# Kernel optimization log

Measured on AMD Instinct MI355X. Metric: run time of the kernel, lower is better.

Reference implementation:

```python
import jax, jax.numpy as jnp
import numpy as np

B, S, D, F, E = 4, 1024, 768, 3072, 8


def setup_inputs() -> dict:
    key = jax.random.key(0)
    k0, k1, k2, k3 = jax.random.split(key, 4)
    hidden_states = jax.random.normal(k0, (B, S, D), dtype=jnp.float32)
    w_router = jax.random.normal(k1, (D, E), dtype=jnp.float32) * 0.02
    w1 = jax.random.normal(k2, (E, D, F), dtype=jnp.float32) * 0.02
    b1 = jnp.zeros((E, F), dtype=jnp.float32)
    w2 = jax.random.normal(k3, (E, F, D), dtype=jnp.float32) * 0.02
    b2 = jnp.zeros((E, D), dtype=jnp.float32)
    return {"hidden_states": hidden_states, "w_router": w_router,
            "w1": w1, "b1": b1, "w2": w2, "b2": b2}


def reference(hidden_states, w_router, w1, b1, w2, b2):
    # Switch-style top-1 router: logits -> softmax -> one-hot mask + max prob
    router_logits = jnp.einsum("bsd,de->bse", hidden_states, w_router)
    router_probs_full = jax.nn.softmax(router_logits, axis=-1)
    expert_index = jnp.argmax(router_probs_full, axis=-1)            # [B,S] int
    router_probs = jnp.max(router_probs_full, axis=-1, keepdims=True)  # [B,S,1]
    router_mask = jax.nn.one_hot(expert_index, E, dtype=hidden_states.dtype)  # [B,S,E]

    # Dispatch/compute/combine: each token goes to exactly one expert FFN.
    # Loop over the small fixed expert set (E=8), combine via the one-hot mask;
    # math is identical to the gather -> expert FFN -> scatter of the original.
    out = jnp.zeros_like(hidden_states)
    for e in range(E):
        h = jax.nn.relu(jnp.einsum("bsd,df->bsf", hidden_states, w1[e]) + b1[e])
        h = jnp.einsum("bsf,fd->bsd", h, w2[e]) + b2[e]
        out = out + router_mask[..., e:e + 1] * h

    hidden_out = router_probs * out  # scale by top-1 router prob, as in original
    return hidden_out, router_logits, expert_index
```

## Files before the change

kernel.cpp:

```cpp
#include <hip/hip_runtime.h>
#include <hip/hip_bf16.h>

#define T_TOK 4096
#define DIM   768
#define FF    3072
#define NE    8
#define MAXTILES 48

typedef __attribute__((ext_vector_type(8))) short bf16x8;
typedef __attribute__((ext_vector_type(4))) short bf16x4;
typedef __attribute__((ext_vector_type(4))) float f32x4;
typedef __attribute__((ext_vector_type(2))) float f32x2;

typedef __attribute__((address_space(1))) void gvoid_t;
typedef __attribute__((address_space(3))) void lvoid_t;

__device__ __forceinline__ void g2l16(const void* g, void* l) {
    __builtin_amdgcn_global_load_lds((gvoid_t*)(void*)g, (lvoid_t*)l, 16, 0, 0);
}

#define WAIT_VM0() __builtin_amdgcn_s_waitcnt(0x0F70)
#define WAIT_VM4() __builtin_amdgcn_s_waitcnt(0x0F74)
#define RAW_BARRIER() asm volatile("s_barrier" ::: "memory")

__device__ __forceinline__ unsigned short f2bf(float f) {
    union { float f; unsigned int u; } v; v.f = f;
    unsigned int u = v.u;
    u += 0x7FFFu + ((u >> 16) & 1u);
    return (unsigned short)(u >> 16);
}

__device__ __forceinline__ bf16x8 pack8(f32x4 a, f32x4 b) {
    bf16x8 r;
    r[0] = (short)f2bf(a[0]); r[1] = (short)f2bf(a[1]);
    r[2] = (short)f2bf(a[2]); r[3] = (short)f2bf(a[3]);
    r[4] = (short)f2bf(b[0]); r[5] = (short)f2bf(b[1]);
    r[6] = (short)f2bf(b[2]); r[7] = (short)f2bf(b[3]);
    return r;
}

__global__ __launch_bounds__(256) void k_router(
    const float* __restrict__ x, const float* __restrict__ wr,
    float* __restrict__ out_logits, float* __restrict__ out_eidx,
    float* __restrict__ probs, int* __restrict__ eidx_i,
    int* __restrict__ counts, int* __restrict__ bucket)
{
    int tok  = (blockIdx.x * 256 + threadIdx.x) >> 6;
    int lane = threadIdx.x & 63;
    if (tok >= T_TOK) return;
    const float* xr = x + (size_t)tok * DIM;
    float acc[NE];
    #pragma unroll
    for (int e = 0; e < NE; e++) acc[e] = 0.f;
    #pragma unroll
    for (int j = 0; j < DIM / 64; j++) {
        int d = j * 64 + lane;
        float xv = xr[d];
        const float* wrow = wr + (size_t)d * NE;
        #pragma unroll
        for (int e = 0; e < NE; e++) acc[e] += xv * wrow[e];
    }
    #pragma unroll
    for (int e = 0; e < NE; e++) {
        #pragma unroll
        for (int off = 32; off >= 1; off >>= 1)
            acc[e] += __shfl_xor(acc[e], off);
    }
    if (lane == 0) {
        float mx = acc[0]; int mi = 0;
        #pragma unroll
        for (int e = 1; e < NE; e++) if (acc[e] > mx) { mx = acc[e]; mi = e; }
        float se = 0.f;
        #pragma unroll
        for (int e = 0; e < NE; e++) se += __expf(acc[e] - mx);
        #pragma unroll
        for (int e = 0; e < NE; e++) out_logits[(size_t)tok * NE + e] = acc[e];
        out_eidx[tok] = (float)mi;
        eidx_i[tok] = mi;
        probs[tok] = 1.f / se;
        int pos = atomicAdd(&counts[mi], 1);
        bucket[mi * T_TOK + pos] = tok;
    }
}

__global__ void k_compact(const int* __restrict__ counts, int* __restrict__ offsets,
                          int* __restrict__ bucket, int* __restrict__ sorted)
{
    __shared__ int soff[NE + 1];
    if (threadIdx.x == 0) {
        int s = 0;
        for (int e = 0; e < NE; e++) { soff[e] = s; s += counts[e]; }
        soff[NE] = s;
        for (int e = 0; e <= NE; e++) offsets[e] = soff[e];
    }
    __syncthreads();
    for (int e = 0; e < NE; e++) {
        int c = counts[e], o = soff[e];
        for (int i = threadIdx.x; i < c; i += blockDim.x)
            sorted[o + i] = bucket[e * T_TOK + i];
    }
    __syncthreads();
    if (threadIdx.x == 0) {
        int nt = 0;
        for (int e = 0; e < NE; e++) {
            int c = counts[e];
            for (int t = 0; t * 128 < c && nt < MAXTILES; t++)
                bucket[nt++] = (e << 8) | t;
        }
        for (int i = nt; i < MAXTILES; i++) bucket[i] = -1;
    }
}

__global__ __launch_bounds__(256) void k_xconv(
    const float* __restrict__ x, unsigned short* __restrict__ Xb)
{
    int g0 = (blockIdx.x * 256 + threadIdx.x) * 8;
    if (g0 >= T_TOK * DIM) return;
    f32x4 a = *(const f32x4*)(x + g0);
    f32x4 b = *(const f32x4*)(x + g0 + 4);
    *(bf16x8*)(Xb + g0) = pack8(a, b);
}

__global__ __launch_bounds__(256) void k_tconv(
    const float* __restrict__ in, unsigned short* __restrict__ out, int R, int C)
{
    const size_t es = (size_t)R * C;
    in  += blockIdx.z * es;
    out += blockIdx.z * es;
    const int c0 = blockIdx.x * 64, r0 = blockIdx.y * 64;
    __shared__ unsigned short t[64][72];
    const int tr = threadIdx.x >> 2, tc = (threadIdx.x & 3) * 16;
    const float* src = in + (size_t)(r0 + tr) * C + c0 + tc;
    f32x4 v0 = *(const f32x4*)(src);
    f32x4 v1 = *(const f32x4*)(src + 4);
    f32x4 v2 = *(const f32x4*)(src + 8);
    f32x4 v3 = *(const f32x4*)(src + 12);
    const int xb = (tc >> 4) & 3;
    const int pr = (((tr >> 3) ^ xb) & 7) * 8 + (tr & 7);
    #pragma unroll
    for (int j = 0; j < 4; j++) {
        t[tc + j][pr]      = f2bf(v0[j]);
        t[tc + 4 + j][pr]  = f2bf(v1[j]);
        t[tc + 8 + j][pr]  = f2bf(v2[j]);
        t[tc + 12 + j][pr] = f2bf(v3[j]);
    }
    __syncthreads();
    const int oc = threadIdx.x >> 2, orr = (threadIdx.x & 3) * 16;
    const int rx = (oc >> 4) & 3;
    const int p0 = ((((orr >> 3) + 0) ^ rx) & 7) * 8;
    const int p1 = ((((orr >> 3) + 1) ^ rx) & 7) * 8;
    bf16x8 o0 = *(const bf16x8*)&t[oc][p0];
    bf16x8 o1 = *(const bf16x8*)&t[oc][p1];
    unsigned short* dst = out + (size_t)(c0 + oc) * R + r0 + orr;
    *(bf16x8*)(dst)     = o0;
    *(bf16x8*)(dst + 8) = o1;
}

__global__ __launch_bounds__(256) void k_fin(
    const float* __restrict__ P, const float* __restrict__ b2,
    const int* __restrict__ eidx, const float* __restrict__ probs,
    float* __restrict__ outh)
{
    const int tok = blockIdx.x;
    const float p = probs[tok];
    const int e = eidx[tok];
    const float* p0 = P + (size_t)tok * DIM;
    const float* p1 = p0 + (size_t)T_TOK * DIM;
    const float* p2 = p1 + (size_t)T_TOK * DIM;
    const float* br = b2 + e * DIM;
    float* o = outh + (size_t)tok * DIM;
    for (int d = threadIdx.x; d < DIM; d += 256)
        o[d] = p * (p0[d] + p1[d] + p2[d] + br[d]);
}

__global__ __launch_bounds__(256, 3) void k_gemm1(
    const unsigned short* __restrict__ Xb, const unsigned short* __restrict__ wt1,
    const float* __restrict__ b1, const int* __restrict__ sorted,
    const int* __restrict__ counts, const int* __restrict__ offsets,
    const int* __restrict__ tile_tab, unsigned short* __restrict__ Hbuf)
{
    const int tv = tile_tab[blockIdx.y];
    if (tv < 0) return;
    const int e  = tv >> 8;
    const int ti = tv & 255;
    const int cnt = counts[e];
    const int n0 = blockIdx.x * 128;
    const int off = offsets[e];
    const int rbase = ti * 128;
    const int tid = threadIdx.x, lane = tid & 63, wave = tid >> 6;
    const int wm = wave >> 1, wn = wave & 1;

    __shared__ unsigned short As[3][128][32];
    __shared__ unsigned short Bs[3][128][32];

    const int lr = lane >> 2;
    const int ls = (lane & 3) * 8;

    int r0 = rbase + wave * 32 + lr;        if (r0 >= cnt) r0 = rbase;
    int r1 = rbase + wave * 32 + 16 + lr;   if (r1 >= cnt) r1 = rbase;
    const unsigned short* aP0 = Xb + (size_t)sorted[off + r0] * DIM + ls;
    const unsigned short* aP1 = Xb + (size_t)sorted[off + r1] * DIM + ls;
    const unsigned short* wB  = wt1 + (size_t)e * FF * DIM;
    const unsigned short* bP0 = wB + (size_t)(n0 + wave * 32 + lr) * DIM + ls;
    const unsigned short* bP1 = wB + (size_t)(n0 + wave * 32 + 16 + lr) * DIM + ls;

    f32x4 acc[4][4];
    #pragma unroll
    for (int i = 0; i < 4; i++)
        #pragma unroll
        for (int j = 0; j < 4; j++) acc[i][j] = (f32x4)0.f;

    const int lrow = lane & 15, kq = lane >> 4;
    const int NIT = DIM / 32;

    g2l16(aP0, &As[0][wave * 32][0]);
    g2l16(aP1, &As[0][wave * 32 + 16][0]);
    g2l16(bP0, &Bs[0][wave * 32][0]);
    g2l16(bP1, &Bs[0][wave * 32 + 16][0]);
    __syncthreads();
    g2l16(aP0 + 32, &As[1][wave * 32][0]);
    g2l16(aP1 + 32, &As[1][wave * 32 + 16][0]);
    g2l16(bP0 + 32, &Bs[1][wave * 32][0]);
    g2l16(bP1 + 32, &Bs[1][wave * 32 + 16][0]);

    for (int it = 0; it < NIT; ++it) {
        const int buf = it % 3;
        if (it > 0) {
            WAIT_VM4();
            RAW_BARRIER();
        }
        if (it + 2 < NIT) {
            const int nb_ = (it + 2) % 3;
            const int ko = (it + 2) * 32;
            g2l16(aP0 + ko, &As[nb_][wave * 32][0]);
            g2l16(aP1 + ko, &As[nb_][wave * 32 + 16][0]);
            g2l16(bP0 + ko, &Bs[nb_][wave * 32][0]);
            g2l16(bP1 + ko, &Bs[nb_][wave * 32 + 16][0]);
        }
        bf16x8 af[4], bfv[4];
        #pragma unroll
        for (int i = 0; i < 4; i++)
            af[i] = *(const bf16x8*)&As[buf][wm * 64 + i * 16 + lrow][kq * 8];
        #pragma unroll
        for (int i = 0; i < 4; i++)
            bfv[i] = *(const bf16x8*)&Bs[buf][wn * 64 + i * 16 + lrow][kq * 8];
        #pragma unroll
        for (int mi = 0; mi < 4; mi++)
            #pragma unroll
            for (int ni = 0; ni < 4; ni++)
                acc[mi][ni] = __builtin_amdgcn_mfma_f32_16x16x32_bf16(
                    af[mi], bfv[ni], acc[mi][ni], 0, 0, 0);
    }

    const int quad = lane >> 4;
    #pragma unroll
    for (int ni = 0; ni < 4; ni++) {
        int gn = n0 + wn * 64 + ni * 16 + lrow;
        float bias = b1[e * FF + gn];
        #pragma unroll
        for (int mi = 0; mi < 4; mi++) {
            f32x4 v = acc[mi][ni];
            #pragma unroll
            for (int r = 0; r < 4; r++) {
                int ml = rbase + wm * 64 + mi * 16 + quad * 4 + r;
                if (ml < cnt) {
                    float h = v[r] + bias; h = h > 0.f ? h : 0.f;
                    Hbuf[(size_t)(off + ml) * FF + gn] = f2bf(h);
                }
            }
        }
    }
}

__global__ __launch_bounds__(256, 3) void k_gemm2(
    const unsigned short* __restrict__ Hbuf, const unsigned short* __restrict__ wt2,
    const int* __restrict__ sorted, const int* __restrict__ counts,
    const int* __restrict__ offsets, const int* __restrict__ tile_tab,
    float* __restrict__ Pbuf)
{
    const int tv = tile_tab[blockIdx.y];
    if (tv < 0) return;
    const int e  = tv >> 8;
    const int ti = tv & 255;
    const int cnt = counts[e];
    const int n0 = blockIdx.x * 128;
    const int kc = blockIdx.z;
    const int off = offsets[e];
    const int rbase = ti * 128;
    const int tid = threadIdx.x, lane = tid & 63, wave = tid >> 6;
    const int wm = wave >> 1, wn = wave & 1;

    __shared__ unsigned short As[3][128][32];
    __shared__ unsigned short Bs[3][128][32];
    __shared__ int s_tok[128];

    if (tid < 128) {
        int rr = rbase + tid; if (rr >= cnt) rr = rbase;
        s_tok[tid] = sorted[off + rr];
    }

    const int lr = lane >> 2, ls = (lane & 3) * 8;
    int r0 = rbase + wave * 32 + lr;        if (r0 >= cnt) r0 = rbase;
    int r1 = rbase + wave * 32 + 16 + lr;   if (r1 >= cnt) r1 = rbase;
    const unsigned short* aP0 = Hbuf + (size_t)(off + r0) * FF + kc * 1024 + ls;
    const unsigned short* aP1 = Hbuf + (size_t)(off + r1) * FF + kc * 1024 + ls;
    const unsigned short* wB  = wt2 + (size_t)e * DIM * FF;
    const unsigned short* bP0 = wB + (size_t)(n0 + wave * 32 + lr) * FF + kc * 1024 + ls;
    const unsigned short* bP1 = wB + (size_t)(n0 + wave * 32 + 16 + lr) * FF + kc * 1024 + ls;

    f32x4 acc[4][4];
    #pragma unroll
    for (int i = 0; i < 4; i++)
        #pragma unroll
        for (int j = 0; j < 4; j++) acc[i][j] = (f32x4)0.f;

    const int lrow = lane & 15, kq = lane >> 4;
    const int NIT = 1024 / 32;

    g2l16(aP0, &As[0][wave * 32][0]);
    g2l16(aP1, &As[0][wave * 32 + 16][0]);
    g2l16(bP0, &Bs[0][wave * 32][0]);
    g2l16(bP1, &Bs[0][wave * 32 + 16][0]);
    __syncthreads();
    g2l16(aP0 + 32, &As[1][wave * 32][0]);
    g2l16(aP1 + 32, &As[1][wave * 32 + 16][0]);
    g2l16(bP0 + 32, &Bs[1][wave * 32][0]);
    g2l16(bP1 + 32, &Bs[1][wave * 32 + 16][0]);

    for (int it = 0; it < NIT; ++it) {
        const int buf = it % 3;
        if (it > 0) {
            WAIT_VM4();
            RAW_BARRIER();
        }
        if (it + 2 < NIT) {
            const int nb_ = (it + 2) % 3;
            const int ko = (it + 2) * 32;
            g2l16(aP0 + ko, &As[nb_][wave * 32][0]);
            g2l16(aP1 + ko, &As[nb_][wave * 32 + 16][0]);
            g2l16(bP0 + ko, &Bs[nb_][wave * 32][0]);
            g2l16(bP1 + ko, &Bs[nb_][wave * 32 + 16][0]);
        }
        bf16x8 af[4], bfv[4];
        #pragma unroll
        for (int i = 0; i < 4; i++)
            af[i] = *(const bf16x8*)&As[buf][wm * 64 + i * 16 + lrow][kq * 8];
        #pragma unroll
        for (int i = 0; i < 4; i++)
            bfv[i] = *(const bf16x8*)&Bs[buf][wn * 64 + i * 16 + lrow][kq * 8];
        #pragma unroll
        for (int mi = 0; mi < 4; mi++)
            #pragma unroll
            for (int ni = 0; ni < 4; ni++)
                acc[mi][ni] = __builtin_amdgcn_mfma_f32_16x16x32_bf16(
                    af[mi], bfv[ni], acc[mi][ni], 0, 0, 0);
    }

    float* Pk = Pbuf + (size_t)kc * T_TOK * DIM;
    const int quad = lane >> 4;
    #pragma unroll
    for (int ni = 0; ni < 4; ni++) {
        int gn = n0 + wn * 64 + ni * 16 + lrow;
        #pragma unroll
        for (int mi = 0; mi < 4; mi++) {
            f32x4 v = acc[mi][ni];
            #pragma unroll
            for (int r = 0; r < 4; r++) {
                int mloc = wm * 64 + mi * 16 + quad * 4 + r;
                if (rbase + mloc < cnt) {
                    Pk[(size_t)s_tok[mloc] * DIM + gn] = v[r];
                }
            }
        }
    }
}

__global__ __launch_bounds__(256) void k_gather_fb(
    const float* __restrict__ x, const int* __restrict__ sorted,
    unsigned short* __restrict__ Xg)
{
    int g0 = (blockIdx.x * 256 + threadIdx.x) * 8;
    if (g0 >= T_TOK * DIM) return;
    int row = g0 / DIM, col = g0 - row * DIM;
    const float* src = x + (size_t)sorted[row] * DIM + col;
    f32x4 a = *(const f32x4*)(src);
    f32x4 b = *(const f32x4*)(src + 4);
    *(bf16x8*)(Xg + (size_t)row * DIM + col) = pack8(a, b);
}

__global__ __launch_bounds__(256, 3) void k_gemm1_fb(
    const unsigned short* __restrict__ Xg, const float* __restrict__ w1,
    const float* __restrict__ b1, const int* __restrict__ counts,
    const int* __restrict__ offsets, unsigned short* __restrict__ Hbuf)
{
    const int e   = blockIdx.y >> 5;
    const int ti  = blockIdx.y & 31;
    const int cnt = counts[e];
    if (ti * 128 >= cnt) return;
    const int n0    = blockIdx.x * 128;
    const int off   = offsets[e];
    const int rbase = ti * 128;
    const int rmax  = cnt - rbase - 1;
    const int tid   = threadIdx.x;
    const int lane  = tid & 63;
    const int wave  = tid >> 6;
    const int wm = wave >> 1, wn = wave & 1;
    __shared__ unsigned short As[128][72];
    __shared__ unsigned short Bs[128][72];
    const float* w1e = w1 + (size_t)e * DIM * FF;
    f32x4 acc[4][4];
    #pragma unroll
    for (int i = 0; i < 4; i++)
        #pragma unroll
        for (int j = 0; j < 4; j++) acc[i][j] = (f32x4)0.f;
    const int arow = tid >> 1, aseg = tid & 1;
    const int are  = (arow <= rmax) ? arow : 0;
    const unsigned short* abase = Xg + (size_t)(off + rbase + are) * DIM + aseg * 32;
    const int kb = tid >> 5, nb = tid & 31;
    const float* bbase = w1e + (size_t)kb * 8 * FF + n0 + nb * 4;
    bf16x8 aR[4];
    f32x4  bR[8];
    #pragma unroll
    for (int j = 0; j < 4; j++) aR[j] = *(const bf16x8*)(abase + j * 8);
    #pragma unroll
    for (int r = 0; r < 8; r++) bR[r] = *(const f32x4*)(bbase + (size_t)r * FF);
    const int lrow = lane & 15, kq = lane >> 4;
    for (int it = 0; it < DIM / 64; ++it) {
        __syncthreads();
        #pragma unroll
        for (int j = 0; j < 4; j++)
            *(bf16x8*)&As[arow][aseg * 32 + j * 8] = aR[j];
        #pragma unroll
        for (int j = 0; j < 4; j++) {
            bf16x8 c;
            #pragma unroll
            for (int r = 0; r < 8; r++) c[r] = (short)f2bf(bR[r][j]);
            *(bf16x8*)&Bs[nb * 4 + j][kb * 8] = c;
        }
        __syncthreads();
        if (it + 1 < DIM / 64) {
            const unsigned short* an = abase + (it + 1) * 64;
            #pragma unroll
            for (int j = 0; j < 4; j++) aR[j] = *(const bf16x8*)(an + j * 8);
            const float* bn = bbase + (size_t)(it + 1) * 64 * FF;
            #pragma unroll
            for (int r = 0; r < 8; r++) bR[r] = *(const f32x4*)(bn + (size_t)r * FF);
        }
        #pragma unroll
        for (int ks = 0; ks < 2; ks++) {
            bf16x8 af[4], bfr[4];
            #pragma unroll
            for (int i = 0; i < 4; i++)
                af[i] = *(const bf16x8*)&As[wm * 64 + i * 16 + lrow][ks * 32 + kq * 8];
            #pragma unroll
            for (int i = 0; i < 4; i++)
                bfr[i] = *(const bf16x8*)&Bs[wn * 64 + i * 16 + lrow][ks * 32 + kq * 8];
            #pragma unroll
            for (int mi = 0; mi < 4; mi++)
                #pragma unroll
                for (int ni = 0; ni < 4; ni++)
                    acc[mi][ni] = __builtin_amdgcn_mfma_f32_16x16x32_bf16(
                        af[mi], bfr[ni], acc[mi][ni], 0, 0, 0);
        }
    }
    const int quad = lane >> 4;
    #pragma unroll
    for (int ni = 0; ni < 4; ni++) {
        int gn = n0 + wn * 64 + ni * 16 + lrow;
        float bias = b1[e * FF + gn];
        #pragma unroll
        for (int mi = 0; mi < 4; mi++) {
            f32x4 v = acc[mi][ni];
            #pragma unroll
            for (int r = 0; r < 4; r++) {
                int ml = wm * 64 + mi * 16 + quad * 4 + r;
                if (rbase + ml < cnt) {
                    float h = v[r] + bias;
                    h = h > 0.f ? h : 0.f;
                    Hbuf[(size_t)(off + rbase + ml) * FF + gn] = f2bf(h);
                }
            }
        }
    }
}

__global__ __launch_bounds__(256, 4) void k_gemm2_fb(
    const unsigned short* __restrict__ Hbuf, const float* __restrict__ w2,
    const float* __restrict__ b2, const int* __restrict__ sorted,
    const int* __restrict__ counts, const int* __restrict__ offsets,
    const float* __restrict__ probs, float* __restrict__ outh)
{
    const int e   = blockIdx.y >> 5;
    const int ti  = blockIdx.y & 31;
    const int cnt = counts[e];
    if (ti * 128 >= cnt) return;
    const int n0    = blockIdx.x * 64;
    const int off   = offsets[e];
    const int rbase = ti * 128;
    const int rmax  = cnt - rbase - 1;
    const int tid   = threadIdx.x;
    const int lane  = tid & 63;
    const int wave  = tid >> 6;
    const int wm = wave >> 1, wn = wave & 1;
    __shared__ unsigned short As[128][72];
    __shared__ unsigned short Bs[64][72];
    __shared__ int   s_tok[128];
    __shared__ float s_prob[128];
    if (tid < 128) {
        int r = rbase + tid;
        int tk = sorted[off + ((r < cnt) ? r : rbase)];
        s_tok[tid]  = tk;
        s_prob[tid] = probs[tk];
    }
    const float* w2e = w2 + (size_t)e * FF * DIM;
    f32x4 acc[4][2];
    #pragma unroll
    for (int i = 0; i < 4; i++)
        #pragma unroll
        for (int j = 0; j < 2; j++) acc[i][j] = (f32x4)0.f;
    const int arow = tid >> 1, aseg = tid & 1;
    const int are  = (arow <= rmax) ? arow : 0;
    const unsigned short* abase = Hbuf + (size_t)(off + rbase + are) * FF + aseg * 32;
    const int kb = tid >> 5, nb = tid & 31;
    const float* bbase = w2e + (size_t)kb * 8 * DIM + n0 + nb * 2;
    bf16x8 aR[4];
    f32x2  bR[8];
    #pragma unroll
    for (int j = 0; j < 4; j++) aR[j] = *(const bf16x8*)(abase + j * 8);
    #pragma unroll
    for (int r = 0; r < 8; r++) bR[r] = *(const f32x2*)(bbase + (size_t)r * DIM);
    const int lrow = lane & 15, kq = lane >> 4;
    for (int it = 0; it < FF / 64; ++it) {
        __syncthreads();
        #pragma unroll
        for (int j = 0; j < 4; j++)
            *(bf16x8*)&As[arow][aseg * 32 + j * 8] = aR[j];
        {
            bf16x8 c0, c1;
            #pragma unroll
            for (int r = 0; r < 8; r++) { c0[r] = (short)f2bf(bR[r][0]); c1[r] = (short)f2bf(bR[r][1]); }
            *(bf16x8*)&Bs[nb * 2 + 0][kb * 8] = c0;
            *(bf16x8*)&Bs[nb * 2 + 1][kb * 8] = c1;
        }
        __syncthreads();
        if (it + 1 < FF / 64) {
            const unsigned short* an = abase + (it + 1) * 64;
            #pragma unroll
            for (int j = 0; j < 4; j++) aR[j] = *(const bf16x8*)(an + j * 8);
            const float* bn = bbase + (size_t)(it + 1) * 64 * DIM;
            #pragma unroll
            for (int r = 0; r < 8; r++) bR[r] = *(const f32x2*)(bn + (size_t)r * DIM);
        }
        #pragma unroll
        for (int ks = 0; ks < 2; ks++) {
            bf16x8 af[4], bfr[2];
            #pragma unroll
            for (int i = 0; i < 4; i++)
                af[i] = *(const bf16x8*)&As[wm * 64 + i * 16 + lrow][ks * 32 + kq * 8];
            #pragma unroll
            for (int i = 0; i < 2; i++)
                bfr[i] = *(const bf16x8*)&Bs[wn * 32 + i * 16 + lrow][ks * 32 + kq * 8];
            #pragma unroll
            for (int mi = 0; mi < 4; mi++)
                #pragma unroll
                for (int ni = 0; ni < 2; ni++)
                    acc[mi][ni] = __builtin_amdgcn_mfma_f32_16x16x32_bf16(
                        af[mi], bfr[ni], acc[mi][ni], 0, 0, 0);
        }
    }
    const int quad = lane >> 4;
    #pragma unroll
    for (int ni = 0; ni < 2; ni++) {
        int gn = n0 + wn * 32 + ni * 16 + lrow;
        float bias = b2[e * DIM + gn];
        #pragma unroll
        for (int mi = 0; mi < 4; mi++) {
            f32x4 v = acc[mi][ni];
            #pragma unroll
            for (int r = 0; r < 4; r++) {
                int ml = wm * 64 + mi * 16 + quad * 4 + r;
                if (rbase + ml < cnt) {
                    outh[(size_t)s_tok[ml] * DIM + gn] = (v[r] + bias) * s_prob[ml];
                }
            }
        }
    }
}

extern "C" void kernel_launch(void* const* d_in, const int* in_sizes, int n_in,
                              void* d_out, int out_size, void* d_ws, size_t ws_size,
                              hipStream_t stream) {
    (void)in_sizes; (void)n_in; (void)out_size;
    const float* x  = (const float*)d_in[0];
    const float* wr = (const float*)d_in[1];
    const float* w1 = (const float*)d_in[2];
    const float* b1 = (const float*)d_in[3];
    const float* w2 = (const float*)d_in[4];
    const float* b2 = (const float*)d_in[5];

    float* out_hidden = (float*)d_out;
    float* out_logits = out_hidden + (size_t)T_TOK * DIM;
    float* out_eidx   = out_logits + (size_t)T_TOK * NE;

    char* ws = (char*)d_ws;
    int*   counts  = (int*)(ws + 0);
    int*   offsets = (int*)(ws + 64);
    float* probs   = (float*)(ws + 128);
    int*   eidx_i  = (int*)(ws + 16512);
    int*   sorted  = (int*)(ws + 32896);
    int*   bucket  = (int*)(ws + 49280);
    int*   tile_tab = bucket;
    unsigned short* Xb   = (unsigned short*)(ws + 180352);
    unsigned short* Hbuf = (unsigned short*)(ws + 6471808);
    unsigned short* wt1  = (unsigned short*)(ws + 31637632);
    unsigned short* wt2  = (unsigned short*)(ws + 69386368);
    float* Pbuf = (float*)(ws + 31637632);
    const size_t NEED = 107135104;

    hipMemsetAsync(counts, 0, 32, stream);
    k_router<<<dim3(T_TOK / 4), dim3(256), 0, stream>>>(
        x, wr, out_logits, out_eidx, probs, eidx_i, counts, bucket);
    k_compact<<<dim3(1), dim3(256), 0, stream>>>(counts, offsets, bucket, sorted);

    if (ws_size >= NEED) {
        k_xconv<<<dim3(T_TOK * DIM / 8 / 256), dim3(256), 0, stream>>>(x, Xb);
        k_tconv<<<dim3(FF / 64, DIM / 64, NE), dim3(256), 0, stream>>>(w1, wt1, DIM, FF);
        k_tconv<<<dim3(DIM / 64, FF / 64, NE), dim3(256), 0, stream>>>(w2, wt2, FF, DIM);
        k_gemm1<<<dim3(FF / 128, MAXTILES), dim3(256), 0, stream>>>(
            Xb, wt1, b1, sorted, counts, offsets, tile_tab, Hbuf);
        k_gemm2<<<dim3(DIM / 128, MAXTILES, 3), dim3(256), 0, stream>>>(
            Hbuf, wt2, sorted, counts, offsets, tile_tab, Pbuf);
        k_fin<<<dim3(T_TOK), dim3(256), 0, stream>>>(
            Pbuf, b2, eidx_i, probs, out_hidden);
    } else {
        k_gather_fb<<<dim3(T_TOK * DIM / 8 / 256), dim3(256), 0, stream>>>(x, sorted, Xb);
        k_gemm1_fb<<<dim3(FF / 128, NE * 32), dim3(256), 0, stream>>>(
            Xb, w1, b1, counts, offsets, Hbuf);
        k_gemm2_fb<<<dim3(DIM / 64, NE * 32), dim3(256), 0, stream>>>(
            Hbuf, w2, b2, sorted, counts, offsets, probs, out_hidden);
    }
}
```

Measured before the change: 376.1 us.

## Widen gemm1 tile to 256 columns and drop split-K in gemm2 with fused epilogue

```diff
diff --git a/kernel.cpp b/kernel.cpp
--- a/kernel.cpp
+++ b/kernel.cpp
@@ -21,6 +21,7 @@
 
 #define WAIT_VM0() __builtin_amdgcn_s_waitcnt(0x0F70)
 #define WAIT_VM4() __builtin_amdgcn_s_waitcnt(0x0F74)
+#define WAIT_VM6() __builtin_amdgcn_s_waitcnt(0x0F76)
 #define RAW_BARRIER() asm volatile("s_barrier" ::: "memory")
 
 __device__ __forceinline__ unsigned short f2bf(float f) {
@@ -156,28 +157,112 @@
     *(bf16x8*)(dst + 8) = o1;
 }
 
-__global__ __launch_bounds__(256) void k_fin(
-    const float* __restrict__ P, const float* __restrict__ b2,
-    const int* __restrict__ eidx, const float* __restrict__ probs,
-    float* __restrict__ outh)
-{
-    const int tok = blockIdx.x;
-    const float p = probs[tok];
-    const int e = eidx[tok];
-    const float* p0 = P + (size_t)tok * DIM;
-    const float* p1 = p0 + (size_t)T_TOK * DIM;
-    const float* p2 = p1 + (size_t)T_TOK * DIM;
-    const float* br = b2 + e * DIM;
-    float* o = outh + (size_t)tok * DIM;
-    for (int d = threadIdx.x; d < DIM; d += 256)
-        o[d] = p * (p0[d] + p1[d] + p2[d] + br[d]);
-}
-
-__global__ __launch_bounds__(256, 3) void k_gemm1(
+__global__ __launch_bounds__(256, 2) void k_gemm1(
     const unsigned short* __restrict__ Xb, const unsigned short* __restrict__ wt1,
     const float* __restrict__ b1, const int* __restrict__ sorted,
     const int* __restrict__ counts, const int* __restrict__ offsets,
     const int* __restrict__ tile_tab, unsigned short* __restrict__ Hbuf)
+{
+    const int tv = tile_tab[blockIdx.y];
+    if (tv < 0) return;
+    const int e  = tv >> 8;
+    const int ti = tv & 255;
+    const int cnt = counts[e];
+    const int n0 = blockIdx.x * 256;
+    const int off = offsets[e];
+    const int rbase = ti * 128;
+    const int tid = threadIdx.x, lane = tid & 63, wave = tid >> 6;
+    const int wm = wave >> 1, wn = wave & 1;
+
+    __shared__ unsigned short As[3][128][32];
+    __shared__ unsigned short Bs[3][256][32];
+
+    const int lr = lane >> 2;
+    const int ls = (lane & 3) * 8;
+
+    int r0 = rbase + wave * 32 + lr;        if (r0 >= cnt) r0 = rbase;
+    int r1 = rbase + wave * 32 + 16 + lr;   if (r1 >= cnt) r1 = rbase;
+    const unsigned short* aP0 = Xb + (size_t)sorted[off + r0] * DIM + ls;
+    const unsigned short* aP1 = Xb + (size_t)sorted[off + r1] * DIM + ls;
+    const unsigned short* wB  = wt1 + (size_t)e * FF * DIM;
+    const unsigned short* bP0 = wB + (size_t)(n0 + wave * 64 +  0 + lr) * DIM + ls;
+    const unsigned short* bP1 = wB + (size_t)(n0 + wave * 64 + 16 + lr) * DIM + ls;
+    const unsigned short* bP2 = wB + (size_t)(n0 + wave * 64 + 32 + lr) * DIM + ls;
+    const unsigned short* bP3 = wB + (size_t)(n0 + wave * 64 + 48 + lr) * DIM + ls;
+
+    f32x4 acc[4][8];
+    #pragma unroll
+    for (int i = 0; i < 4; i++)
+        #pragma unroll
+        for (int j = 0; j < 8; j++) acc[i][j] = (f32x4)0.f;
+
+    const int lrow = lane & 15, kq = lane >> 4;
+    const int NIT = DIM / 32;
+
+#define STAGE1(bufi, ko) do { \
+    g2l16(aP0 + (ko), &As[bufi][wave * 32][0]);       \
+    g2l16(aP1 + (ko), &As[bufi][wave * 32 + 16][0]);  \
+    g2l16(bP0 + (ko), &Bs[bufi][wave * 64][0]);       \
+    g2l16(bP1 + (ko), &Bs[bufi][wave * 64 + 16][0]);  \
+    g2l16(bP2 + (ko), &Bs[bufi][wave * 64 + 32][0]);  \
+    g2l16(bP3 + (ko), &Bs[bufi][wave * 64 + 48][0]);  \
+} while (0)
+
+    STAGE1(0, 0);
+    __syncthreads();
+    STAGE1(1, 32);
+
+    for (int it = 0; it < NIT; ++it) {
+        const int buf = it % 3;
+        if (it > 0) {
+            if (it + 1 < NIT) WAIT_VM6(); else WAIT_VM0();
+            RAW_BARRIER();
+        }
+        if (it + 2 < NIT) {
+            STAGE1((it + 2) % 3, (it + 2) * 32);
+        }
+        bf16x8 af[4], bfv[8];
+        #pragma unroll
+        for (int i = 0; i < 4; i++)
+            af[i] = *(const bf16x8*)&As[buf][wm * 64 + i * 16 + lrow][kq * 8];
+        #pragma unroll
+        for (int j = 0; j < 8; j++)
+            bfv[j] = *(const bf16x8*)&Bs[buf][wn * 128 + j * 16 + lrow][kq * 8];
+        #pragma unroll
+        for (int mi = 0; mi < 4; mi++)
+            #pragma unroll
+            for (int ni = 0; ni < 8; ni++)
+                acc[mi][ni] = __builtin_amdgcn_mfma_f32_16x16x32_bf16(
+                    af[mi], bfv[ni], acc[mi][ni], 0, 0, 0);
+    }
+#undef STAGE1
+
+    const int quad = lane >> 4;
+    #pragma unroll
+    for (int ni = 0; ni < 8; ni++) {
+        int gn = n0 + wn * 128 + ni * 16 + lrow;
+        float bias = b1[e * FF + gn];
+        #pragma unroll
+        for (int mi = 0; mi < 4; mi++) {
+            f32x4 v = acc[mi][ni];
+            #pragma unroll
+            for (int r = 0; r < 4; r++) {
+                int ml = rbase + wm * 64 + mi * 16 + quad * 4 + r;
+                if (ml < cnt) {
+                    float h = v[r] + bias; h = h > 0.f ? h : 0.f;
+                    Hbuf[(size_t)(off + ml) * FF + gn] = f2bf(h);
+                }
+            }
+        }
+    }
+}
+
+__global__ __launch_bounds__(256, 3) void k_gemm2(
+    const unsigned short* __restrict__ Hbuf, const unsigned short* __restrict__ wt2,
+    const float* __restrict__ b2, const int* __restrict__ sorted,
+    const int* __restrict__ counts, const int* __restrict__ offsets,
+    const int* __restrict__ tile_tab, const float* __restrict__ probs,
+    float* __restrict__ outh)
 {
     const int tv = tile_tab[blockIdx.y];
     if (tv < 0) return;
@@ -192,17 +277,24 @@
 
     __shared__ unsigned short As[3][128][32];
     __shared__ unsigned short Bs[3][128][32];
-
-    const int lr = lane >> 2;
-    const int ls = (lane & 3) * 8;
-
+    __shared__ int   s_tok[128];
+    __shared__ float s_prob[128];
+
+    if (tid < 128) {
+        int rr = rbase + tid; if (rr >= cnt) rr = rbase;
+        int tk = sorted[off + rr];
+        s_tok[tid]  = tk;
+        s_prob[tid] = probs[tk];
+    }
+
+    const int lr = lane >> 2, ls = (lane & 3) * 8;
     int r0 = rbase + wave * 32 + lr;        if (r0 >= cnt) r0 = rbase;
     int r1 = rbase + wave * 32 + 16 + lr;   if (r1 >= cnt) r1 = rbase;
-    const unsigned short* aP0 = Xb + (size_t)sorted[off + r0] * DIM + ls;
-    const unsigned short* aP1 = Xb + (size_t)sorted[off + r1] * DIM + ls;
-    const unsigned short* wB  = wt1 + (size_t)e * FF * DIM;
-    const unsigned short* bP0 = wB + (size_t)(n0 + wave * 32 + lr) * DIM + ls;
-    const unsigned short* bP1 = wB + (size_t)(n0 + wave * 32 + 16 + lr) * DIM + ls;
+    const unsigned short* aP0 = Hbuf + (size_t)(off + r0) * FF + ls;
+    const unsigned short* aP1 = Hbuf + (size_t)(off + r1) * FF + ls;
+    const unsigned short* wB  = wt2 + (size_t)e * DIM * FF;
+    const unsigned short* bP0 = wB + (size_t)(n0 + wave * 32 + lr) * FF + ls;
+    const unsigned short* bP1 = wB + (size_t)(n0 + wave * 32 + 16 + lr) * FF + ls;
 
     f32x4 acc[4][4];
     #pragma unroll
@@ -211,31 +303,27 @@
         for (int j = 0; j < 4; j++) acc[i][j] = (f32x4)0.f;
 
     const int lrow = lane & 15, kq = lane >> 4;
-    const int NIT = DIM / 32;
-
-    g2l16(aP0, &As[0][wave * 32][0]);
-    g2l16(aP1, &As[0][wave * 32 + 16][0]);
-    g2l16(bP0, &Bs[0][wave * 32][0]);
-    g2l16(bP1, &Bs[0][wave * 32 + 16][0]);
+    const int NIT = FF / 32;
+
+#define STAGE2(bufi, ko) do { \
+    g2l16(aP0 + (ko), &As[bufi][wave * 32][0]);       \
+    g2l16(aP1 + (ko), &As[bufi][wave * 32 + 16][0]);  \
+    g2l16(bP0 + (ko), &Bs[bufi][wave * 32][0]);       \
+    g2l16(bP1 + (ko), &Bs[bufi][wave * 32 + 16][0]);  \
+} while (0)
+
+    STAGE2(0, 0);
     __syncthreads();
-    g2l16(aP0 + 32, &As[1][wave * 32][0]);
-    g2l16(aP1 + 32, &As[1][wave * 32 + 16][0]);
-    g2l16(bP0 + 32, &Bs[1][wave * 32][0]);
-    g2l16(bP1 + 32, &Bs[1][wave * 32 + 16][0]);
+    STAGE2(1, 32);
 
     for (int it = 0; it < NIT; ++it) {
         const int buf = it % 3;
         if (it > 0) {
-            WAIT_VM4();
+            if (it + 1 < NIT) WAIT_VM4(); else WAIT_VM0();
             RAW_BARRIER();
         }
         if (it + 2 < NIT) {
-            const int nb_ = (it + 2) % 3;
-            const int ko = (it + 2) * 32;
-            g2l16(aP0 + ko, &As[nb_][wave * 32][0]);
-            g2l16(aP1 + ko, &As[nb_][wave * 32 + 16][0]);
-            g2l16(bP0 + ko, &Bs[nb_][wave * 32][0]);
-            g2l16(bP1 + ko, &Bs[nb_][wave * 32 + 16][0]);
+            STAGE2((it + 2) % 3, (it + 2) * 32);
         }
         bf16x8 af[4], bfv[4];
         #pragma unroll
@@ -251,116 +339,13 @@
                 acc[mi][ni] = __builtin_amdgcn_mfma_f32_16x16x32_bf16(
                     af[mi], bfv[ni], acc[mi][ni], 0, 0, 0);
     }
+#undef STAGE2
 
     const int quad = lane >> 4;
     #pragma unroll
     for (int ni = 0; ni < 4; ni++) {
         int gn = n0 + wn * 64 + ni * 16 + lrow;
-        float bias = b1[e * FF + gn];
-        #pragma unroll
-        for (int mi = 0; mi < 4; mi++) {
-            f32x4 v = acc[mi][ni];
-            #pragma unroll
-            for (int r = 0; r < 4; r++) {
-                int ml = rbase + wm * 64 + mi * 16 + quad * 4 + r;
-                if (ml < cnt) {
-                    float h = v[r] + bias; h = h > 0.f ? h : 0.f;
-                    Hbuf[(size_t)(off + ml) * FF + gn] = f2bf(h);
-                }
-            }
-        }
-    }
-}
-
-__global__ __launch_bounds__(256, 3) void k_gemm2(
-    const unsigned short* __restrict__ Hbuf, const unsigned short* __restrict__ wt2,
-    const int* __restrict__ sorted, const int* __restrict__ counts,
-    const int* __restrict__ offsets, const int* __restrict__ tile_tab,
-    float* __restrict__ Pbuf)
-{
-    const int tv = tile_tab[blockIdx.y];
-    if (tv < 0) return;
-    const int e  = tv >> 8;
-    const int ti = tv & 255;
-    const int cnt = counts[e];
-    const int n0 = blockIdx.x * 128;
-    const int kc = blockIdx.z;
-    const int off = offsets[e];
-    const int rbase = ti * 128;
-    const int tid = threadIdx.x, lane = tid & 63, wave = tid >> 6;
-    const int wm = wave >> 1, wn = wave & 1;
-
-    __shared__ unsigned short As[3][128][32];
-    __shared__ unsigned short Bs[3][128][32];
-    __shared__ int s_tok[128];
-
-    if (tid < 128) {
-        int rr = rbase + tid; if (rr >= cnt) rr = rbase;
-        s_tok[tid] = sorted[off + rr];
-    }
-
-    const int lr = lane >> 2, ls = (lane & 3) * 8;
-    int r0 = rbase + wave * 32 + lr;        if (r0 >= cnt) r0 = rbase;
-    int r1 = rbase + wave * 32 + 16 + lr;   if (r1 >= cnt) r1 = rbase;
-    const unsigned short* aP0 = Hbuf + (size_t)(off + r0) * FF + kc * 1024 + ls;
-    const unsigned short* aP1 = Hbuf + (size_t)(off + r1) * FF + kc * 1024 + ls;
-    const unsigned short* wB  = wt2 + (size_t)e * DIM * FF;
-    const unsigned short* bP0 = wB + (size_t)(n0 + wave * 32 + lr) * FF + kc * 1024 + ls;
-    const unsigned short* bP1 = wB + (size_t)(n0 + wave * 32 + 16 + lr) * FF + kc * 1024 + ls;
-
-    f32x4 acc[4][4];
-    #pragma unroll
-    for (int i = 0; i < 4; i++)
-        #pragma unroll
-        for (int j = 0; j < 4; j++) acc[i][j] = (f32x4)0.f;
-
-    const int lrow = lane & 15, kq = lane >> 4;
-    const int NIT = 1024 / 32;
-
-    g2l16(aP0, &As[0][wave * 32][0]);
-    g2l16(aP1, &As[0][wave * 32 + 16][0]);
-    g2l16(bP0, &Bs[0][wave * 32][0]);
-    g2l16(bP1, &Bs[0][wave * 32 + 16][0]);
-    __syncthreads();
-    g2l16(aP0 + 32, &As[1][wave * 32][0]);
-    g2l16(aP1 + 32, &As[1][wave * 32 + 16][0]);
-    g2l16(bP0 + 32, &Bs[1][wave * 32][0]);
-    g2l16(bP1 + 32, &Bs[1][wave * 32 + 16][0]);
-
-    for (int it = 0; it < NIT; ++it) {
-        const int buf = it % 3;
-        if (it > 0) {
-            WAIT_VM4();
-            RAW_BARRIER();
-        }
-        if (it + 2 < NIT) {
-            const int nb_ = (it + 2) % 3;
-            const int ko = (it + 2) * 32;
-            g2l16(aP0 + ko, &As[nb_][wave * 32][0]);
-            g2l16(aP1 + ko, &As[nb_][wave * 32 + 16][0]);
-            g2l16(bP0 + ko, &Bs[nb_][wave * 32][0]);
-            g2l16(bP1 + ko, &Bs[nb_][wave * 32 + 16][0]);
-        }
-        bf16x8 af[4], bfv[4];
-        #pragma unroll
-        for (int i = 0; i < 4; i++)
-            af[i] = *(const bf16x8*)&As[buf][wm * 64 + i * 16 + lrow][kq * 8];
-        #pragma unroll
-        for (int i = 0; i < 4; i++)
-            bfv[i] = *(const bf16x8*)&Bs[buf][wn * 64 + i * 16 + lrow][kq * 8];
-        #pragma unroll
-        for (int mi = 0; mi < 4; mi++)
-            #pragma unroll
-            for (int ni = 0; ni < 4; ni++)
-                acc[mi][ni] = __builtin_amdgcn_mfma_f32_16x16x32_bf16(
-                    af[mi], bfv[ni], acc[mi][ni], 0, 0, 0);
-    }
-
-    float* Pk = Pbuf + (size_t)kc * T_TOK * DIM;
-    const int quad = lane >> 4;
-    #pragma unroll
-    for (int ni = 0; ni < 4; ni++) {
-        int gn = n0 + wn * 64 + ni * 16 + lrow;
+        float bias = b2[e * DIM + gn];
         #pragma unroll
         for (int mi = 0; mi < 4; mi++) {
             f32x4 v = acc[mi][ni];
@@ -368,7 +353,7 @@
             for (int r = 0; r < 4; r++) {
                 int mloc = wm * 64 + mi * 16 + quad * 4 + r;
                 if (rbase + mloc < cnt) {
-                    Pk[(size_t)s_tok[mloc] * DIM + gn] = v[r];
+                    outh[(size_t)s_tok[mloc] * DIM + gn] = (v[r] + bias) * s_prob[mloc];
                 }
             }
         }
@@ -614,7 +599,6 @@
     unsigned short* Hbuf = (unsigned short*)(ws + 6471808);
     unsigned short* wt1  = (unsigned short*)(ws + 31637632);
     unsigned short* wt2  = (unsigned short*)(ws + 69386368);
-    float* Pbuf = (float*)(ws + 31637632);
     const size_t NEED = 107135104;
 
     hipMemsetAsync(counts, 0, 32, stream);
@@ -626,12 +610,10 @@
         k_xconv<<<dim3(T_TOK * DIM / 8 / 256), dim3(256), 0, stream>>>(x, Xb);
         k_tconv<<<dim3(FF / 64, DIM / 64, NE), dim3(256), 0, stream>>>(w1, wt1, DIM, FF);
         k_tconv<<<dim3(DIM / 64, FF / 64, NE), dim3(256), 0, stream>>>(w2, wt2, FF, DIM);
-        k_gemm1<<<dim3(FF / 128, MAXTILES), dim3(256), 0, stream>>>(
+        k_gemm1<<<dim3(FF / 256, MAXTILES), dim3(256), 0, stream>>>(
             Xb, wt1, b1, sorted, counts, offsets, tile_tab, Hbuf);
-        k_gemm2<<<dim3(DIM / 128, MAXTILES, 3), dim3(256), 0, stream>>>(
-            Hbuf, wt2, sorted, counts, offsets, tile_tab, Pbuf);
-        k_fin<<<dim3(T_TOK), dim3(256), 0, stream>>>(
-            Pbuf, b2, eidx_i, probs, out_hidden);
+        k_gemm2<<<dim3(DIM / 128, MAXTILES), dim3(256), 0, stream>>>(
+            Hbuf, wt2, b2, sorted, counts, offsets, tile_tab, probs, out_hidden);
     } else {
         k_gather_fb<<<dim3(T_TOK * DIM / 8 / 256), dim3(256), 0, stream>>>(x, sorted, Xb);
         k_gemm1_fb<<<dim3(FF / 128, NE * 32), dim3(256), 0, stream>>>(
```

New measurement: 389.9 us. 1.04x slower.
